# Kernel optimization log

Hardware: AMD Instinct MI355X
Metric: run time of the kernel (lower is better)

Reference implementation:

```python
import jax, jax.numpy as jnp
import numpy as np
from jax import lax

D = 4            # shift radius
NSHIFT = 2 * D + 1  # 9 shifts per axis -> 81 total


def setup_inputs() -> dict:
    key = jax.random.key(0)
    k1, k2, k3, k4, k5, k6 = jax.random.split(key, 6)
    B, C, H, W = 4, 256, 64, 128
    R = 16  # reduction ratio
    feat1 = jax.random.normal(k1, (B, C, H, W), dtype=jnp.float32)
    feat2 = jax.random.normal(k2, (B, C, H, W), dtype=jnp.float32)
    # ca_conv1: Conv2d(C, C//R, 1) -> weight [C//R, C], bias [C//R]
    w1 = jax.random.normal(k3, (C // R, C), dtype=jnp.float32) * (1.0 / np.sqrt(C))
    b1 = jax.random.normal(k4, (C // R,), dtype=jnp.float32) * 0.01
    # ca_conv2: Conv2d(C//R, C, 1) -> weight [C, C//R], bias [C]
    w2 = jax.random.normal(k5, (C, C // R), dtype=jnp.float32) * (1.0 / np.sqrt(C // R))
    b2 = jax.random.normal(k6, (C,), dtype=jnp.float32) * 0.01
    return {"feat1": feat1, "feat2": feat2, "w1": w1, "b1": b1, "w2": w2, "b2": b2}


def reference(feat1, feat2, w1, b1, w2, b2):
    B, C, H, W = feat1.shape
    # zero-pad feat2 spatially by D on each side (matches F.pad constant 0)
    feat2p = jnp.pad(feat2, ((0, 0), (0, 0), (D, D), (D, D)))

    def one_shift(carry, idx):
        i = idx // NSHIFT
        j = idx % NSHIFT
        f2 = lax.dynamic_slice(feat2p, (0, 0, i, j), (B, C, H, W))
        sim = feat1 * f2                              # [B,C,H,W]
        pooled = jnp.mean(sim, axis=(2, 3))           # global avg pool -> [B,C]
        a = pooled @ w1.T + b1                        # [B,C//R] (1x1 conv == matmul)
        a = a @ w2.T + b2                             # [B,C]
        a = jax.nn.sigmoid(a)
        out = jnp.mean(a[:, :, None, None] * sim, axis=1)  # channel mean -> [B,H,W]
        return carry, out

    _, cv = lax.scan(one_shift, None, jnp.arange(NSHIFT * NSHIFT))  # [81,B,H,W]
    return jnp.transpose(cv, (1, 0, 2, 3))  # [B,81,H,W]
```

## Files before the change

### kernel.cpp

```cpp
#include <hip/hip_runtime.h>
#include <math.h>


#define HH 64
#define WW 128
#define CC 256
#define BB 4

__global__ __launch_bounds__(576) void corr_pool_kernel(
    const float* __restrict__ f1, const float* __restrict__ f2,
    float* __restrict__ pooled) {
  const int t  = threadIdx.x;
  const int bc = blockIdx.x;
  const float* f1p = f1 + (size_t)bc * (HH * WW);
  const float* f2p = f2 + (size_t)bc * (HH * WW);

  __shared__ float4 f2s4[72 * 35];

  const float4 z4 = make_float4(0.f, 0.f, 0.f, 0.f);
  for (int u = t; u < 72 * 35; u += 576) {
    const int rl = u / 35, k = u - rl * 35;
    const int gr = rl - 4;
    float4 v = z4;
    if ((unsigned)gr < 64u && k >= 1 && k <= 32)
      v = *(const float4*)(f2p + (gr << 7) + ((k - 1) << 2));
    f2s4[u] = v;
  }
  __syncthreads();

  const int h  = t / 9;
  const int di = t - h * 9;
  const float4* f2row = &f2s4[(h + di) * 35];
  const float* f1row  = f1p + (h << 7);

  float s9[9];
#pragma unroll
  for (int j = 0; j < 9; ++j) s9[j] = 0.f;

  alignas(16) float f1c[16], f2wc[24];
#pragma unroll
  for (int m = 0; m < 4; ++m)
    *(float4*)&f1c[4 * m] = *(const float4*)(f1row + (m << 2));
#pragma unroll
  for (int m = 0; m < 6; ++m) *(float4*)&f2wc[4 * m] = f2row[m];

  for (int seg = 0; seg < 8; ++seg) {
    const int nxt = (seg < 7) ? seg + 1 : 7;
    alignas(16) float f1n[16], f2wn[24];
#pragma unroll
    for (int m = 0; m < 4; ++m)
      *(float4*)&f1n[4 * m] =
          *(const float4*)(f1row + (nxt << 4) + (m << 2));
#pragma unroll
    for (int m = 0; m < 6; ++m) *(float4*)&f2wn[4 * m] = f2row[(nxt << 2) + m];

#pragma unroll
    for (int k = 0; k < 16; ++k) {
      const float a = f1c[k];
#pragma unroll
      for (int j = 0; j < 9; ++j) s9[j] += a * f2wc[k + j];
    }
#pragma unroll
    for (int m = 0; m < 16; ++m) f1c[m] = f1n[m];
#pragma unroll
    for (int m = 0; m < 24; ++m) f2wc[m] = f2wn[m];
  }

  __syncthreads();
  float* red  = (float*)f2s4;
  float* red2 = red + 64 * 81;
#pragma unroll
  for (int j = 0; j < 9; ++j) red[h * 81 + di * 9 + j] = s9[j];
  __syncthreads();

  if (t < 567) {
    const int col = t % 81, g = t / 81;
    const int r0 = g * 9, r1 = (g == 6) ? 64 : r0 + 9;
    float acc = 0.f;
#pragma unroll 3
    for (int rr = r0; rr < r1; ++rr) acc += red[rr * 81 + col];
    red2[g * 81 + col] = acc;
  }
  __syncthreads();

  if (t < 81) {
    float acc = 0.f;
#pragma unroll
    for (int g = 0; g < 7; ++g) acc += red2[g * 81 + t];
    const int b = bc >> 8, c = bc & 255;
    pooled[(size_t)(b * 81 + t) * 256 + c] = acc;
  }
}

__global__ __launch_bounds__(256) void mlp_kernel(
    const float* __restrict__ pooled, const float* __restrict__ w1,
    const float* __restrict__ b1, const float* __restrict__ w2,
    const float* __restrict__ b2, float* __restrict__ At) {
  const int bs = blockIdx.x;
  const int t  = threadIdx.x;
  const int b  = bs / 81;
  const int s  = bs - b * 81;
  __shared__ float p[256];
  __shared__ float hid[16];

  p[t] = pooled[(size_t)bs * 256 + t] * (1.0f / 8192.0f);
  __syncthreads();

  const int g = t >> 4, ln = t & 15;
  float acc = 0.f;
#pragma unroll
  for (int m = 0; m < 16; ++m) {
    const int c = (m << 4) + ln;
    acc += w1[(g << 8) + c] * p[c];
  }
  acc += __shfl_xor(acc, 1);
  acc += __shfl_xor(acc, 2);
  acc += __shfl_xor(acc, 4);
  acc += __shfl_xor(acc, 8);
  if (ln == 0) hid[g] = acc + b1[g];
  __syncthreads();

  float acc2 = b2[t];
#pragma unroll
  for (int k = 0; k < 16; ++k) acc2 += w2[(t << 4) + k] * hid[k];
  const float sv = 1.0f / (1.0f + __expf(-acc2));
  At[((size_t)(b * 256 + t)) * 81 + s] = sv;
}

__global__ __launch_bounds__(64, 4) void out_kernel(
    const float* __restrict__ f1, const float* __restrict__ f2,
    const float* __restrict__ At, float* __restrict__ out,
    float* __restrict__ part) {
  const int bid  = blockIdx.x;
  const int x    = bid & 7;
  const int q    = bid >> 3;
  const int i    = q % 9;
  const int tq   = q / 9;
  const int tile = tq * 8 + x;
  const int half = tile & 1;
  const int rt   = (tile >> 1) & 31;
  const int b    = tile >> 6;
  const int h0   = rt << 1;

  const int t    = threadIdx.x;
  const int r    = t >> 5;
  const int cidx = t & 31;
  const int w0   = cidx << 2;
  const int h    = h0 + r;
  const int hr   = h + i - 4;
  const bool rowok = ((unsigned)hr < 64u);

  float acc[9][4];
#pragma unroll
  for (int j = 0; j < 9; ++j)
#pragma unroll
    for (int k = 0; k < 4; ++k) acc[j][k] = 0.f;

  if (rowok) {
    const int c0 = half << 7;
    const float* p1 = f1 + (size_t)b * (CC * 8192) + (size_t)c0 * 8192 +
                      (h << 7) + w0;
    const float* p2 = f2 + (size_t)b * (CC * 8192) + (size_t)c0 * 8192 +
                      (hr << 7);
    const float* Ab = At + (size_t)b * (CC * 81) + (size_t)c0 * 81 + i * 9;

    const bool vA  = (cidx > 0);
    const bool vC  = (cidx < 31);
    const int ofsA = vA ? (w0 - 4) : 0;
    const int ofsC = vC ? (w0 + 4) : 120;

    float4 s0x = *(const float4*)(p1);
    float4 s0A = *(const float4*)(p2 + ofsA);
    float4 s0B = *(const float4*)(p2 + w0);
    float4 s0C = *(const float4*)(p2 + ofsC);
    p1 += 8192; p2 += 8192;
    float4 s1x = *(const float4*)(p1);
    float4 s1A = *(const float4*)(p2 + ofsA);
    float4 s1B = *(const float4*)(p2 + w0);
    float4 s1C = *(const float4*)(p2 + ofsC);

    float av[9];
#pragma unroll
    for (int j = 0; j < 9; ++j) av[j] = Ab[j];
    const float* qa = Ab + 81;

    for (int c = 0; c < 128; ++c) {
      const int adv = (c < 126) ? 8192 : 0;
      p1 += adv; p2 += adv;
      const float4 nx = *(const float4*)(p1);
      const float4 nA = *(const float4*)(p2 + ofsA);
      const float4 nB = *(const float4*)(p2 + w0);
      const float4 nC = *(const float4*)(p2 + ofsC);

      float avn[9];
#pragma unroll
      for (int j = 0; j < 9; ++j) avn[j] = qa[j];

      alignas(16) float f2r[12];
      f2r[0] = vA ? s0A.x : 0.f;
      f2r[1] = vA ? s0A.y : 0.f;
      f2r[2] = vA ? s0A.z : 0.f;
      f2r[3] = vA ? s0A.w : 0.f;
      f2r[4] = s0B.x; f2r[5] = s0B.y; f2r[6] = s0B.z; f2r[7] = s0B.w;
      f2r[8]  = vC ? s0C.x : 0.f;
      f2r[9]  = vC ? s0C.y : 0.f;
      f2r[10] = vC ? s0C.z : 0.f;
      f2r[11] = vC ? s0C.w : 0.f;

      alignas(16) const float xx[4] = {s0x.x, s0x.y, s0x.z, s0x.w};

#pragma unroll
      for (int j = 0; j < 9; ++j) {
        const float wj = av[j];
#pragma unroll
        for (int k = 0; k < 4; ++k) acc[j][k] += wj * (xx[k] * f2r[k + j]);
      }

      s0x = s1x; s0A = s1A; s0B = s1B; s0C = s1C;
      s1x = nx;  s1A = nA;  s1B = nB;  s1C = nC;
#pragma unroll
      for (int j = 0; j < 9; ++j) av[j] = avn[j];
      qa += (c < 126) ? 81 : 0;
    }
  }

  float* dst = half ? part : out;
  const float inv = 1.0f / 256.0f;
#pragma unroll
  for (int j = 0; j < 9; ++j) {
    float4 o;
    o.x = acc[j][0] * inv;
    o.y = acc[j][1] * inv;
    o.z = acc[j][2] * inv;
    o.w = acc[j][3] * inv;
    *(float4*)(dst + (((size_t)(b * 81 + i * 9 + j) * 64 + h) << 7) + w0) = o;
  }
}

__global__ __launch_bounds__(256) void combine_kernel(
    float* __restrict__ out, const float* __restrict__ part) {
  const size_t idx = (size_t)blockIdx.x * 256 + threadIdx.x;
  float4* o4       = (float4*)out;
  const float4* p4 = (const float4*)part;
  const float4 a = o4[idx], p = p4[idx];
  float4 rv;
  rv.x = a.x + p.x; rv.y = a.y + p.y; rv.z = a.z + p.z; rv.w = a.w + p.w;
  o4[idx] = rv;
}

extern "C" void kernel_launch(void* const* d_in, const int* in_sizes, int n_in,
                              void* d_out, int out_size, void* d_ws, size_t ws_size,
                              hipStream_t stream) {
  const float* feat1 = (const float*)d_in[0];
  const float* feat2 = (const float*)d_in[1];
  const float* w1    = (const float*)d_in[2];
  const float* b1    = (const float*)d_in[3];
  const float* w2    = (const float*)d_in[4];
  const float* b2    = (const float*)d_in[5];
  float* out = (float*)d_out;

  float* pooled = (float*)d_ws;
  float* At     = pooled + 82944;
  float* cpart  = At + 82944;

  corr_pool_kernel<<<1024, 576, 0, stream>>>(feat1, feat2, pooled);
  mlp_kernel<<<4 * 81, 256, 0, stream>>>(pooled, w1, b1, w2, b2, At);
  out_kernel<<<2304, 64, 0, stream>>>(feat1, feat2, At, out, cpart);
  combine_kernel<<<2592, 256, 0, stream>>>(out, cpart);
}
```

Baseline: 197.8 us.

## Stage feat1/feat2 row tiles in shared memory across all nine vertical shifts

```diff
diff --git a/kernel.cpp b/kernel.cpp
--- a/kernel.cpp
+++ b/kernel.cpp
@@ -127,28 +127,55 @@
   At[((size_t)(b * 256 + t)) * 81 + s] = sv;
 }
 
-__global__ __launch_bounds__(64, 4) void out_kernel(
+#define SCH 4
+__global__ __launch_bounds__(576) void out_kernel(
     const float* __restrict__ f1, const float* __restrict__ f2,
     const float* __restrict__ At, float* __restrict__ out,
     float* __restrict__ part) {
   const int bid  = blockIdx.x;
-  const int x    = bid & 7;
-  const int q    = bid >> 3;
-  const int i    = q % 9;
-  const int tq   = q / 9;
-  const int tile = tq * 8 + x;
-  const int half = tile & 1;
-  const int rt   = (tile >> 1) & 31;
-  const int b    = tile >> 6;
+  const int half = bid & 1;
+  const int rt   = (bid >> 1) & 31;
+  const int b    = bid >> 6;
   const int h0   = rt << 1;
 
   const int t    = threadIdx.x;
-  const int r    = t >> 5;
-  const int cidx = t & 31;
+  const int i    = t >> 6;
+  const int l    = t & 63;
+  const int r    = l >> 5;
+  const int cidx = l & 31;
   const int w0   = cidx << 2;
   const int h    = h0 + r;
-  const int hr   = h + i - 4;
-  const bool rowok = ((unsigned)hr < 64u);
+
+  __shared__ float4 sbuf[2][SCH * 404];
+
+  const int c0 = half << 7;
+  const float* f1b = f1 + ((size_t)b * CC + c0) * 8192;
+  const float* f2b = f2 + ((size_t)b * CC + c0) * 8192;
+  const float* Ab  = At + ((size_t)b * CC + c0) * 81 + i * 9;
+
+  const float4 z4 = make_float4(0.f, 0.f, 0.f, 0.f);
+
+  auto stage = [&](int g, int buf) {
+    const int cg = g * SCH;
+    for (int u = t; u < SCH * 404; u += 576) {
+      const int cc  = u / 404;
+      const int rem = u - cc * 404;
+      float4 v = z4;
+      if (rem < 340) {
+        const int rr = rem / 34, kk = rem - rr * 34;
+        const int gr = h0 + rr - 4;
+        if ((unsigned)gr < 64u && kk >= 1 && kk <= 32)
+          v = *(const float4*)(f2b + (size_t)(cg + cc) * 8192 + (gr << 7) +
+                               ((kk - 1) << 2));
+      } else {
+        const int idx = rem - 340;
+        const int fr = idx >> 5, k2 = idx & 31;
+        v = *(const float4*)(f1b + (size_t)(cg + cc) * 8192 +
+                             ((h0 + fr) << 7) + (k2 << 2));
+      }
+      sbuf[buf][u] = v;
+    }
+  };
 
   float acc[9][4];
 #pragma unroll
@@ -156,72 +183,36 @@
 #pragma unroll
     for (int k = 0; k < 4; ++k) acc[j][k] = 0.f;
 
-  if (rowok) {
-    const int c0 = half << 7;
-    const float* p1 = f1 + (size_t)b * (CC * 8192) + (size_t)c0 * 8192 +
-                      (h << 7) + w0;
-    const float* p2 = f2 + (size_t)b * (CC * 8192) + (size_t)c0 * 8192 +
-                      (hr << 7);
-    const float* Ab = At + (size_t)b * (CC * 81) + (size_t)c0 * 81 + i * 9;
-
-    const bool vA  = (cidx > 0);
-    const bool vC  = (cidx < 31);
-    const int ofsA = vA ? (w0 - 4) : 0;
-    const int ofsC = vC ? (w0 + 4) : 120;
-
-    float4 s0x = *(const float4*)(p1);
-    float4 s0A = *(const float4*)(p2 + ofsA);
-    float4 s0B = *(const float4*)(p2 + w0);
-    float4 s0C = *(const float4*)(p2 + ofsC);
-    p1 += 8192; p2 += 8192;
-    float4 s1x = *(const float4*)(p1);
-    float4 s1A = *(const float4*)(p2 + ofsA);
-    float4 s1B = *(const float4*)(p2 + w0);
-    float4 s1C = *(const float4*)(p2 + ofsC);
-
-    float av[9];
-#pragma unroll
-    for (int j = 0; j < 9; ++j) av[j] = Ab[j];
-    const float* qa = Ab + 81;
-
-    for (int c = 0; c < 128; ++c) {
-      const int adv = (c < 126) ? 8192 : 0;
-      p1 += adv; p2 += adv;
-      const float4 nx = *(const float4*)(p1);
-      const float4 nA = *(const float4*)(p2 + ofsA);
-      const float4 nB = *(const float4*)(p2 + w0);
-      const float4 nC = *(const float4*)(p2 + ofsC);
-
-      float avn[9];
-#pragma unroll
-      for (int j = 0; j < 9; ++j) avn[j] = qa[j];
+  stage(0, 0);
+  __syncthreads();
+
+  for (int g = 0; g < 32; ++g) {
+    if (g < 31) stage(g + 1, (g + 1) & 1);
+
+    const float4* cb = &sbuf[g & 1][0];
+#pragma unroll
+    for (int cc = 0; cc < SCH; ++cc) {
+      const float4* chb = cb + cc * 404;
+      const float4 f1v = chb[340 + (r << 5) + cidx];
+      const float4 q0  = chb[(r + i) * 34 + cidx];
+      const float4 q1  = chb[(r + i) * 34 + cidx + 1];
+      const float4 q2  = chb[(r + i) * 34 + cidx + 2];
 
       alignas(16) float f2r[12];
-      f2r[0] = vA ? s0A.x : 0.f;
-      f2r[1] = vA ? s0A.y : 0.f;
-      f2r[2] = vA ? s0A.z : 0.f;
-      f2r[3] = vA ? s0A.w : 0.f;
-      f2r[4] = s0B.x; f2r[5] = s0B.y; f2r[6] = s0B.z; f2r[7] = s0B.w;
-      f2r[8]  = vC ? s0C.x : 0.f;
-      f2r[9]  = vC ? s0C.y : 0.f;
-      f2r[10] = vC ? s0C.z : 0.f;
-      f2r[11] = vC ? s0C.w : 0.f;
-
-      alignas(16) const float xx[4] = {s0x.x, s0x.y, s0x.z, s0x.w};
-
+      *(float4*)&f2r[0] = q0;
+      *(float4*)&f2r[4] = q1;
+      *(float4*)&f2r[8] = q2;
+      alignas(16) const float xx[4] = {f1v.x, f1v.y, f1v.z, f1v.w};
+
+      const float* av = Ab + (size_t)(g * SCH + cc) * 81;
 #pragma unroll
       for (int j = 0; j < 9; ++j) {
         const float wj = av[j];
 #pragma unroll
         for (int k = 0; k < 4; ++k) acc[j][k] += wj * (xx[k] * f2r[k + j]);
       }
-
-      s0x = s1x; s0A = s1A; s0B = s1B; s0C = s1C;
-      s1x = nx;  s1A = nA;  s1B = nB;  s1C = nC;
-#pragma unroll
-      for (int j = 0; j < 9; ++j) av[j] = avn[j];
-      qa += (c < 126) ? 81 : 0;
     }
+    __syncthreads();
   }
 
   float* dst = half ? part : out;
@@ -265,6 +256,6 @@
 
   corr_pool_kernel<<<1024, 576, 0, stream>>>(feat1, feat2, pooled);
   mlp_kernel<<<4 * 81, 256, 0, stream>>>(pooled, w1, b1, w2, b2, At);
-  out_kernel<<<2304, 64, 0, stream>>>(feat1, feat2, At, out, cpart);
+  out_kernel<<<256, 576, 0, stream>>>(feat1, feat2, At, out, cpart);
   combine_kernel<<<2592, 256, 0, stream>>>(out, cpart);
 }
```

After: 224.5 us. 13.5% more time.
